# Optimization experiments

Measured on AMD Instinct MI355X. Metric: run time of the kernel, lower is better.

Reference implementation:

```python
import jax, jax.numpy as jnp
import numpy as np

E = 1024
H = 16
HD = 64
DI = E // 16  # 64, GRU hidden size
VOCAB = 32000
B, T = 2, 2048


def adaptive_pool_matrix(l_in, l_out):
    # PyTorch AdaptiveAvgPool1d: out[i] = mean(in[floor(i*l_in/l_out) : ceil((i+1)*l_in/l_out)])
    P = np.zeros((l_in, l_out), np.float32)
    for i in range(l_out):
        s = (i * l_in) // l_out
        e = -((-(i + 1) * l_in) // l_out)
        P[s:e, i] = 1.0 / (e - s)
    return jnp.asarray(P)


def gru(x, wih, whh):
    # x: [B, T, DI]; wih/whh: [3*DI, DI]; no bias; gate order (r, z, n)
    h_dim = whh.shape[1]
    xw = jnp.einsum('btd,gd->btg', x, wih)  # [B, T, 3*DI]

    def step(h, xw_t):
        hw = h @ whh.T
        r = jax.nn.sigmoid(xw_t[:, :h_dim] + hw[:, :h_dim])
        z = jax.nn.sigmoid(xw_t[:, h_dim:2 * h_dim] + hw[:, h_dim:2 * h_dim])
        n = jnp.tanh(xw_t[:, 2 * h_dim:] + r * hw[:, 2 * h_dim:])
        h_new = (1.0 - z) * n + z * h
        return h_new, h_new

    h0 = jnp.zeros((x.shape[0], h_dim), x.dtype)
    _, hs = jax.lax.scan(step, h0, jnp.swapaxes(xw, 0, 1))
    return jnp.swapaxes(hs, 0, 1)  # [B, T, DI]


def pos_embed(x, gru_wih, gru_whh, lin_w, p_pos, p_proj):
    # x: [B, T, E]. Pools act on the feature dim (torch last-dim after permute).
    x_proj = x @ p_proj            # [B, T, E-DI]
    pos = gru(x @ p_pos, gru_wih, gru_whh)  # [B, T, DI]
    out = jnp.concatenate([pos, x_proj], axis=-1) @ lin_w.T
    return out + x


def layernorm(x, w, b, eps=1e-5):
    mu = jnp.mean(x, axis=-1, keepdims=True)
    var = jnp.var(x, axis=-1, keepdims=True)
    return (x - mu) * jax.lax.rsqrt(var + eps) * w + b


def setup_inputs() -> dict:
    key = jax.random.key(0)
    ks = jax.random.split(key, 16)
    s = 0.02
    return {
        'x': jax.random.normal(ks[0], (B, T, E), jnp.float32),
        'token_ids': jax.random.randint(ks[1], (B, T), 0, VOCAB, jnp.int32),
        'q_gru_wih': jax.random.normal(ks[2], (3 * DI, DI), jnp.float32) * s,
        'q_gru_whh': jax.random.normal(ks[3], (3 * DI, DI), jnp.float32) * s,
        'q_lin_w': jax.random.normal(ks[4], (E, E), jnp.float32) * s,
        'k_gru_wih': jax.random.normal(ks[5], (3 * DI, DI), jnp.float32) * s,
        'k_gru_whh': jax.random.normal(ks[6], (3 * DI, DI), jnp.float32) * s,
        'k_lin_w': jax.random.normal(ks[7], (E, E), jnp.float32) * s,
        'v_emb': jax.random.normal(ks[8], (VOCAB, E), jnp.float32) * s + 1.0,
        'q_ln_w': jnp.ones((E,), jnp.float32),
        'q_ln_b': jnp.zeros((E,), jnp.float32),
        'k_ln_w': jnp.ones((E,), jnp.float32),
        'k_ln_b': jnp.zeros((E,), jnp.float32),
        'out_w': jax.random.normal(ks[9], (E, E), jnp.float32) * s,
        'out_b': jnp.zeros((E,), jnp.float32),
    }


def reference(x, token_ids, q_gru_wih, q_gru_whh, q_lin_w, k_gru_wih, k_gru_whh,
              k_lin_w, v_emb, q_ln_w, q_ln_b, k_ln_w, k_ln_b, out_w, out_b):
    p_pos = adaptive_pool_matrix(E, DI)
    p_proj = adaptive_pool_matrix(E, E - DI)

    q = pos_embed(x, q_gru_wih, q_gru_whh, q_lin_w, p_pos, p_proj)
    k = pos_embed(x, k_gru_wih, k_gru_whh, k_lin_w, p_pos, p_proj)
    v = jax.nn.silu(x) * v_emb[token_ids]  # [B, T, E]

    q = layernorm(q, q_ln_w, q_ln_b)
    k = layernorm(k, k_ln_w, k_ln_b)

    # [B, T, E] -> [B, H, T, HD]
    def split_heads(t):
        return t.reshape(B, T, H, HD).transpose(0, 2, 1, 3)

    qh, kh, vh = split_heads(q), split_heads(k), split_heads(v)

    scores = jnp.einsum('bhtd,bhsd->bhts', qh, kh) / jnp.sqrt(jnp.float32(HD))
    # Original code: attn_weights += attn_weights.masked_fill(mask, -inf)
    # => unmasked scores are DOUBLED; masked (future) positions become -inf.
    causal = jnp.triu(jnp.ones((T, T), bool), k=1)  # True above diagonal
    scores = jnp.where(causal, -jnp.inf, scores * 2.0)
    attn = jax.nn.softmax(scores, axis=-1)

    out = jnp.einsum('bhts,bhsd->bhtd', attn, vh)  # [B, H, T, HD]
    out = out.transpose(0, 2, 1, 3).reshape(B, T, E)
    return out @ out_w.T + out_b
```

## Files before the change

kernel.cpp:

```cpp
#include <hip/hip_runtime.h>


namespace {

constexpr int B_ = 2, T_ = 2048, E_ = 1024, H_ = 16, HD_ = 64, G3_ = 192, M_ = B_ * T_;

typedef _Float16 f16;
typedef _Float16 f16x8 __attribute__((ext_vector_type(8)));
typedef _Float16 f16x4 __attribute__((ext_vector_type(4)));
typedef _Float16 f16x2 __attribute__((ext_vector_type(2)));
typedef float f32x4 __attribute__((ext_vector_type(4)));

__device__ __forceinline__ f32x4 mfma16(f16x8 a, f16x8 b, f32x4 c) {
  return __builtin_amdgcn_mfma_f32_16x16x32_f16(a, b, c, 0, 0, 0);
}

#if __has_builtin(__builtin_amdgcn_fdot2)
__device__ __forceinline__ float fdot2(f16x2 a, f16x2 b, float c) {
  return __builtin_amdgcn_fdot2(a, b, c, false);
}
#else
__device__ __forceinline__ float fdot2(f16x2 a, f16x2 b, float c) {
  return c + (float)a[0] * (float)b[0] + (float)a[1] * (float)b[1];
}
#endif

__global__ __launch_bounds__(256) void k_cvt(const float* __restrict__ s,
                                             f16* __restrict__ d, int n) {
  int i = (blockIdx.x * 256 + threadIdx.x) * 4;
  if (i < n) {
    float4 v = *(const float4*)(s + i);
    f16x4 o = {(f16)v.x, (f16)v.y, (f16)v.z, (f16)v.w};
    *(f16x4*)(d + i) = o;
  }
}

__global__ __launch_bounds__(256) void k_prep(
    const float* __restrict__ x, const int* __restrict__ tok,
    const f16* __restrict__ wihq, const f16* __restrict__ wihk,
    const float* __restrict__ v_emb,
    f16* __restrict__ vh, f16* __restrict__ aq, f16* __restrict__ ak,
    float* __restrict__ xwq, float* __restrict__ xwk) {
  __shared__ float xs[E_];
  __shared__ float xp[64];
  const int row = blockIdx.x;
  const int b = row >> 11, t = row & (T_ - 1);
  const int tid = threadIdx.x;
  const float* xrow = x + (size_t)row * E_;
  {
    const int tk = tok[row];
    float4 xv = ((const float4*)xrow)[tid];
    ((float4*)xs)[tid] = xv;
    float4 ev = ((const float4*)(v_emb + (size_t)tk * E_))[tid];
    f16x4 o;
    o[0] = (f16)(xv.x / (1.f + __expf(-xv.x)) * ev.x);
    o[1] = (f16)(xv.y / (1.f + __expf(-xv.y)) * ev.y);
    o[2] = (f16)(xv.z / (1.f + __expf(-xv.z)) * ev.z);
    o[3] = (f16)(xv.w / (1.f + __expf(-xv.w)) * ev.w);
    const int e0 = tid * 4;
    const size_t voff = ((size_t)(b * H_ + (e0 >> 6)) * T_ + t) * HD_ + (e0 & 63);
    *(f16x4*)(vh + voff) = o;
  }
  __syncthreads();
  if (tid < 64) {
    float s = 0.f;
#pragma unroll
    for (int j = 0; j < 16; ++j) s += xs[tid * 16 + j];
    xp[tid] = s * (1.f / 16.f);
  }
  for (int i = tid; i < 960; i += 256) {
    int s0 = (i * 1024) / 960;
    int e0 = ((i + 1) * 1024 + 959) / 960;
    float m = xs[s0];
    if (e0 - s0 == 2) m = (m + xs[s0 + 1]) * 0.5f;
    f16 hv = (f16)m;
    aq[(size_t)row * E_ + 64 + i] = hv;
    ak[(size_t)row * E_ + 64 + i] = hv;
  }
  __syncthreads();
  for (int o = tid; o < 2 * G3_; o += 256) {
    const int chain = o / G3_, g = o % G3_;
    const f16* wrow = (chain ? wihk : wihq) + g * 64;
    float acc = 0.f;
#pragma unroll
    for (int c = 0; c < 8; ++c) {
      f16x8 wv = *(const f16x8*)(wrow + c * 8);
#pragma unroll
      for (int u = 0; u < 8; ++u) acc += xp[c * 8 + u] * (float)wv[u];
    }
    (chain ? xwk : xwq)[(size_t)row * G3_ + g] = acc;
  }
}

__global__ __launch_bounds__(64, 1) void k_gru(
    const float* __restrict__ xwq, const float* __restrict__ xwk,
    const float* __restrict__ whhq, const float* __restrict__ whhk,
    f16* __restrict__ aq, f16* __restrict__ ak) {
  const int blk = blockIdx.x;
  const int chain = blk >> 1, b = blk & 1;
  const float* xw = (chain ? xwk : xwq) + (size_t)b * T_ * G3_;
  const float* whh = chain ? whhk : whhq;
  f16* a = (chain ? ak : aq) + (size_t)b * T_ * E_;
  const int j = threadIdx.x;
  f16x2 wr2[32], wz2[32], wn2[32];
#pragma unroll
  for (int i = 0; i < 32; ++i) {
    float2 r2 = *(const float2*)(whh + (size_t)j * 64 + 2 * i);
    float2 z2 = *(const float2*)(whh + (size_t)(64 + j) * 64 + 2 * i);
    float2 n2 = *(const float2*)(whh + (size_t)(128 + j) * 64 + 2 * i);
    wr2[i] = {(f16)r2.x, (f16)r2.y};
    wz2[i] = {(f16)z2.x, (f16)z2.y};
    wn2[i] = {(f16)n2.x, (f16)n2.y};
  }
  float h = 0.f;
  float xr = xw[j], xz = xw[64 + j], xn = xw[128 + j];
  for (int t = 0; t < T_; ++t) {
    const f16 h16 = (f16)h;
    const unsigned hu = (unsigned)__builtin_bit_cast(unsigned short, h16);
    const unsigned nb = (unsigned)__shfl_xor((int)hu, 1) & 0xffffu;
    const unsigned pk = (j & 1) ? (nb | (hu << 16)) : (hu | (nb << 16));
    int hp[32];
#pragma unroll
    for (int i = 0; i < 32; ++i) hp[i] = __builtin_amdgcn_readlane((int)pk, 2 * i);
    const int tn = (t + 1 < T_) ? (t + 1) : (T_ - 1);
    const float* xp2 = xw + (size_t)tn * G3_;
    const float nxr = xp2[j], nxz = xp2[64 + j], nxn = xp2[128 + j];
    float ar = 0.f, az = 0.f, an = 0.f;
#pragma unroll
    for (int i = 0; i < 32; ++i) {
      const f16x2 hh = __builtin_bit_cast(f16x2, hp[i]);
      ar = fdot2(wr2[i], hh, ar);
      az = fdot2(wz2[i], hh, az);
      an = fdot2(wn2[i], hh, an);
    }
    const float r = 1.f / (1.f + __expf(-(xr + ar)));
    const float z = 1.f / (1.f + __expf(-(xz + az)));
    const float pre = xn + r * an;
    const float ea = __expf(-2.f * fabsf(pre));
    float nn = (1.f - ea) / (1.f + ea);
    nn = copysignf(nn, pre);
    h = (1.f - z) * nn + z * h;
    a[(size_t)t * E_ + j] = (f16)h;
    xr = nxr; xz = nxz; xn = nxn;
  }
}

template <int MODE>
__global__ __launch_bounds__(256) void k_gemm(
    const f16* __restrict__ A, const f16* __restrict__ W,
    const float* __restrict__ add, const float* __restrict__ bias,
    float* __restrict__ C) {
  __shared__ __align__(16) f16 As[128][72];
  __shared__ __align__(16) f16 Bs[128][72];
  const int m0 = blockIdx.x * 128, n0 = blockIdx.y * 128;
  const int tid = threadIdx.x;
  const int wid = tid >> 6, lane = tid & 63;
  const int wr = wid >> 1, wc = wid & 1;
  const int lg = lane >> 4, lc = lane & 15;
  f32x4 acc[4][4] = {};
  for (int kt = 0; kt < E_; kt += 64) {
#pragma unroll
    for (int it = 0; it < 4; ++it) {
      const int r = it * 32 + (tid >> 3);
      const int cs = (tid & 7) * 8;
      *(f16x8*)&As[r][cs] = *(const f16x8*)(A + (size_t)(m0 + r) * E_ + kt + cs);
      *(f16x8*)&Bs[r][cs] = *(const f16x8*)(W + (size_t)(n0 + r) * E_ + kt + cs);
    }
    __syncthreads();
    f16x8 af[4][2], bf[4][2];
#pragma unroll
    for (int mi = 0; mi < 4; ++mi)
#pragma unroll
      for (int ks = 0; ks < 2; ++ks) {
        af[mi][ks] = *(const f16x8*)&As[wr * 64 + mi * 16 + lc][ks * 32 + lg * 8];
        bf[mi][ks] = *(const f16x8*)&Bs[wc * 64 + mi * 16 + lc][ks * 32 + lg * 8];
      }
#pragma unroll
    for (int mi = 0; mi < 4; ++mi)
#pragma unroll
      for (int ni = 0; ni < 4; ++ni)
#pragma unroll
        for (int ks = 0; ks < 2; ++ks)
          acc[mi][ni] = mfma16(af[mi][ks], bf[ni][ks], acc[mi][ni]);
    __syncthreads();
  }
#pragma unroll
  for (int mi = 0; mi < 4; ++mi) {
    const int r0 = m0 + wr * 64 + mi * 16 + lg * 4;
#pragma unroll
    for (int ni = 0; ni < 4; ++ni) {
      const int col = n0 + wc * 64 + ni * 16 + lc;
      const float bv = (MODE == 1) ? bias[col] : 0.f;
#pragma unroll
      for (int q = 0; q < 4; ++q) {
        float v = acc[mi][ni][q];
        if (MODE == 0) v += add[(size_t)(r0 + q) * E_ + col];
        else v += bv;
        C[(size_t)(r0 + q) * E_ + col] = v;
      }
    }
  }
}

__global__ __launch_bounds__(256) void k_ln(const float* __restrict__ pre,
                                            const float* __restrict__ gw,
                                            const float* __restrict__ gb,
                                            f16* __restrict__ outp) {
  const int row = blockIdx.x;
  const int tid = threadIdx.x;
  const float4 v = ((const float4*)(pre + (size_t)row * E_))[tid];
  float s = v.x + v.y + v.z + v.w;
  float s2 = v.x * v.x + v.y * v.y + v.z * v.z + v.w * v.w;
#pragma unroll
  for (int off = 32; off; off >>= 1) {
    s += __shfl_xor(s, off);
    s2 += __shfl_xor(s2, off);
  }
  __shared__ float red[8];
  const int wid = tid >> 6, lane = tid & 63;
  if (!lane) { red[wid] = s; red[4 + wid] = s2; }
  __syncthreads();
  s = red[0] + red[1] + red[2] + red[3];
  s2 = red[4] + red[5] + red[6] + red[7];
  const float mu = s * (1.f / E_);
  const float inv = rsqrtf(s2 * (1.f / E_) - mu * mu + 1e-5f);
  const float4 w4 = ((const float4*)gw)[tid];
  const float4 b4 = ((const float4*)gb)[tid];
  const int e0 = tid * 4;
  f16x4 o;
  o[0] = (f16)((v.x - mu) * inv * w4.x + b4.x);
  o[1] = (f16)((v.y - mu) * inv * w4.y + b4.y);
  o[2] = (f16)((v.z - mu) * inv * w4.z + b4.z);
  o[3] = (f16)((v.w - mu) * inv * w4.w + b4.w);
  const int b = row >> 11, t = row & (T_ - 1);
  const size_t off2 = ((size_t)(b * H_ + (e0 >> 6)) * T_ + t) * HD_ + (e0 & 63);
  *(f16x4*)(outp + off2) = o;
}

__global__ __launch_bounds__(256) void k_attn(const f16* __restrict__ Q,
                                              const f16* __restrict__ K,
                                              const f16* __restrict__ V,
                                              f16* __restrict__ AO) {
  __shared__ __align__(16) f16 Kt[64][72];
  __shared__ __align__(16) f16 Vt[64][72];
  __shared__ __align__(16) f16 Ps[4][16][72];
  const int qi = blockIdx.x, bh = blockIdx.y;
  const int b = bh >> 4, h = bh & 15;
  const int tid = threadIdx.x, wid = tid >> 6, lane = tid & 63;
  const int lg = lane >> 4, lc = lane & 15;
  const size_t hbase = (size_t)bh * T_ * HD_;
  const int qb = qi * 64;
  f16x8 qf[2];
  {
    const int qrow = qb + wid * 16 + lc;
#pragma unroll
    for (int ks = 0; ks < 2; ++ks)
      qf[ks] = *(const f16x8*)(Q + hbase + (size_t)qrow * HD_ + ks * 32 + lg * 8);
  }
  f32x4 o[4] = {};
  float m_run[4] = {-1e30f, -1e30f, -1e30f, -1e30f};
  float l_run[4] = {};
  const int qrow_d = qb + wid * 16 + lg * 4;
  for (int kt = 0; kt <= qi; ++kt) {
    {
      const int r = tid >> 2, cs = (tid & 3) * 16;
      const f16* ksrc = K + hbase + (size_t)(kt * 64 + r) * HD_ + cs;
      *(f16x8*)&Kt[r][cs] = *(const f16x8*)ksrc;
      *(f16x8*)&Kt[r][cs + 8] = *(const f16x8*)(ksrc + 8);
      const f16* vsrc = V + hbase + (size_t)(kt * 64 + lane) * HD_ + wid * 16;
      f16x8 va = *(const f16x8*)vsrc;
      f16x8 vb = *(const f16x8*)(vsrc + 8);
#pragma unroll
      for (int u = 0; u < 8; ++u) {
        Vt[wid * 16 + u][lane] = va[u];
        Vt[wid * 16 + 8 + u][lane] = vb[u];
      }
    }
    __syncthreads();
    f32x4 s[4] = {};
#pragma unroll
    for (int nt = 0; nt < 4; ++nt)
#pragma unroll
      for (int ks = 0; ks < 2; ++ks) {
        f16x8 kf = *(const f16x8*)&Kt[nt * 16 + lc][ks * 32 + lg * 8];
        s[nt] = mfma16(qf[ks], kf, s[nt]);
      }
    const bool diag = (kt == qi);
#pragma unroll
    for (int nt = 0; nt < 4; ++nt) {
      const int colg = kt * 64 + nt * 16 + lc;
#pragma unroll
      for (int r = 0; r < 4; ++r) {
        float v = s[nt][r] * 0.25f;
        if (diag && colg > qrow_d + r) v = -1e30f;
        s[nt][r] = v;
      }
    }
    float scalev[4];
#pragma unroll
    for (int r = 0; r < 4; ++r) {
      float m = fmaxf(fmaxf(s[0][r], s[1][r]), fmaxf(s[2][r], s[3][r]));
#pragma unroll
      for (int of = 1; of < 16; of <<= 1) m = fmaxf(m, __shfl_xor(m, of));
      const float mn = fmaxf(m_run[r], m);
      scalev[r] = __expf(m_run[r] - mn);
      m_run[r] = mn;
    }
    float ladd[4] = {};
#pragma unroll
    for (int nt = 0; nt < 4; ++nt)
#pragma unroll
      for (int r = 0; r < 4; ++r) {
        const float p = __expf(s[nt][r] - m_run[r]);
        s[nt][r] = p;
        ladd[r] += p;
      }
#pragma unroll
    for (int r = 0; r < 4; ++r) {
      float la = ladd[r];
#pragma unroll
      for (int of = 1; of < 16; of <<= 1) la += __shfl_xor(la, of);
      l_run[r] = l_run[r] * scalev[r] + la;
      o[0][r] *= scalev[r];
      o[1][r] *= scalev[r];
      o[2][r] *= scalev[r];
      o[3][r] *= scalev[r];
    }
#pragma unroll
    for (int nt = 0; nt < 4; ++nt)
#pragma unroll
      for (int r = 0; r < 4; ++r)
        Ps[wid][lg * 4 + r][nt * 16 + lc] = (f16)s[nt][r];
    f16x8 pf[2];
#pragma unroll
    for (int ks = 0; ks < 2; ++ks)
      pf[ks] = *(const f16x8*)&Ps[wid][lc][ks * 32 + lg * 8];
#pragma unroll
    for (int nt = 0; nt < 4; ++nt)
#pragma unroll
      for (int ks = 0; ks < 2; ++ks) {
        f16x8 vf = *(const f16x8*)&Vt[nt * 16 + lc][ks * 32 + lg * 8];
        o[nt] = mfma16(pf[ks], vf, o[nt]);
      }
    __syncthreads();
  }
#pragma unroll
  for (int nt = 0; nt < 4; ++nt)
#pragma unroll
    for (int r = 0; r < 4; ++r) {
      const float val = o[nt][r] / l_run[r];
      const int qrow = qrow_d + r;
      AO[((size_t)(b * T_ + qrow)) * E_ + h * HD_ + nt * 16 + lc] = (f16)val;
    }
}

}

extern "C" void kernel_launch(void* const* d_in, const int* in_sizes, int n_in,
                              void* d_out, int out_size, void* d_ws, size_t ws_size,
                              hipStream_t stream) {
  (void)in_sizes; (void)n_in; (void)out_size; (void)ws_size;
  const float* x      = (const float*)d_in[0];
  const int*   tok    = (const int*)d_in[1];
  const float* q_wih  = (const float*)d_in[2];
  const float* q_whh  = (const float*)d_in[3];
  const float* q_lin  = (const float*)d_in[4];
  const float* k_wih  = (const float*)d_in[5];
  const float* k_whh  = (const float*)d_in[6];
  const float* k_lin  = (const float*)d_in[7];
  const float* v_emb  = (const float*)d_in[8];
  const float* q_ln_w = (const float*)d_in[9];
  const float* q_ln_b = (const float*)d_in[10];
  const float* k_ln_w = (const float*)d_in[11];
  const float* k_ln_b = (const float*)d_in[12];
  const float* out_w  = (const float*)d_in[13];
  const float* out_b  = (const float*)d_in[14];
  float* outp = (float*)d_out;

  char* ws = (char*)d_ws;
  size_t off = 0;
  auto take = [&](size_t bytes) -> void* {
    void* p = ws + off;
    off += (bytes + 255) & ~(size_t)255;
    return p;
  };
  f16* WQ   = (f16*)take((size_t)E_ * E_ * 2);
  f16* WK   = (f16*)take((size_t)E_ * E_ * 2);
  f16* WO   = (f16*)take((size_t)E_ * E_ * 2);
  f16* WIHQ = (f16*)take((size_t)G3_ * 64 * 2);
  f16* WIHK = (f16*)take((size_t)G3_ * 64 * 2);
  f16* AQ   = (f16*)take((size_t)M_ * E_ * 2);
  f16* AK   = (f16*)take((size_t)M_ * E_ * 2);
  f16* VH   = (f16*)take((size_t)M_ * E_ * 2);
  f16* QH   = (f16*)take((size_t)M_ * E_ * 2);
  f16* KH   = (f16*)take((size_t)M_ * E_ * 2);
  f16* AO   = (f16*)take((size_t)M_ * E_ * 2);
  float* XWQ  = (float*)take((size_t)M_ * G3_ * 4);
  float* XWK  = (float*)take((size_t)M_ * G3_ * 4);
  float* QPRE = (float*)take((size_t)M_ * E_ * 4);
  float* KPRE = (float*)take((size_t)M_ * E_ * 4);

  k_cvt<<<dim3((E_ * E_) / 1024), dim3(256), 0, stream>>>(q_lin, WQ, E_ * E_);
  k_cvt<<<dim3((E_ * E_) / 1024), dim3(256), 0, stream>>>(k_lin, WK, E_ * E_);
  k_cvt<<<dim3((E_ * E_) / 1024), dim3(256), 0, stream>>>(out_w, WO, E_ * E_);
  k_cvt<<<dim3((G3_ * 64) / 1024), dim3(256), 0, stream>>>(q_wih, WIHQ, G3_ * 64);
  k_cvt<<<dim3((G3_ * 64) / 1024), dim3(256), 0, stream>>>(k_wih, WIHK, G3_ * 64);

  k_prep<<<dim3(M_), dim3(256), 0, stream>>>(x, tok, WIHQ, WIHK, v_emb, VH, AQ, AK, XWQ, XWK);
  k_gru<<<dim3(4), dim3(64), 0, stream>>>(XWQ, XWK, q_whh, k_whh, AQ, AK);

  k_gemm<0><<<dim3(M_ / 128, E_ / 128), dim3(256), 0, stream>>>(AQ, WQ, x, nullptr, QPRE);
  k_gemm<0><<<dim3(M_ / 128, E_ / 128), dim3(256), 0, stream>>>(AK, WK, x, nullptr, KPRE);
  k_ln<<<dim3(M_), dim3(256), 0, stream>>>(QPRE, q_ln_w, q_ln_b, QH);
  k_ln<<<dim3(M_), dim3(256), 0, stream>>>(KPRE, k_ln_w, k_ln_b, KH);

  k_attn<<<dim3(T_ / 64, B_ * H_), dim3(256), 0, stream>>>(QH, KH, VH, AO);
  k_gemm<1><<<dim3(M_ / 128, E_ / 128), dim3(256), 0, stream>>>(AO, WO, nullptr, out_b, outp);
}
```

Baseline: 1.084 ms.

## Overlap GRU recurrence with pooled-feature GEMM in one mega kernel

Merges the serial GRU scan with the Q/K projection GEMMs and the out_w fp16 conversion into one launch. Block 0 runs all four GRU chains as four waves, while the other blocks compute the GEMM over the K range that skips the first 64 GRU columns. A later k_fix kernel adds the GRU-column contribution and the residual x. The GRU step is also reworked: gate weights are prescaled so sigmoid/tanh become exp2 plus rcp, lanes are broadcast via permlane32 swap, and the three dot products are reordered to shorten the dependency chain. The Q/K LayerNorms are batched into one launch. The cost is an extra read-modify-write pass over QPRE/KPRE and a dependence on GEMM blocks co-running with the long GRU block, since k_mega does not return until the GRU finishes.

```diff
diff --git a/kernel.cpp b/kernel.cpp
--- a/kernel.cpp
+++ b/kernel.cpp
@@ -4,6 +4,8 @@
 namespace {
 
 constexpr int B_ = 2, T_ = 2048, E_ = 1024, H_ = 16, HD_ = 64, G3_ = 192, M_ = B_ * T_;
+constexpr float SRg = -1.4426950408889634f;
+constexpr float SNg = 2.8853900817779268f;
 
 typedef _Float16 f16;
 typedef _Float16 f16x8 __attribute__((ext_vector_type(8)));
@@ -24,6 +26,21 @@
   return c + (float)a[0] * (float)b[0] + (float)a[1] * (float)b[1];
 }
 #endif
+
+__device__ __forceinline__ float exp2_(float x) {
+#if __has_builtin(__builtin_amdgcn_exp2f)
+  return __builtin_amdgcn_exp2f(x);
+#else
+  return exp2f(x);
+#endif
+}
+__device__ __forceinline__ float rcp_(float x) {
+#if __has_builtin(__builtin_amdgcn_rcpf)
+  return __builtin_amdgcn_rcpf(x);
+#else
+  return 1.f / x;
+#endif
+}
 
 __global__ __launch_bounds__(256) void k_cvt(const float* __restrict__ s,
                                              f16* __restrict__ d, int n) {
@@ -88,124 +105,204 @@
 #pragma unroll
       for (int u = 0; u < 8; ++u) acc += xp[c * 8 + u] * (float)wv[u];
     }
-    (chain ? xwk : xwq)[(size_t)row * G3_ + g] = acc;
-  }
-}
-
-__global__ __launch_bounds__(64, 1) void k_gru(
+    const float sc = (g < 128) ? SRg : SNg;
+    (chain ? xwk : xwq)[(size_t)row * G3_ + g] = acc * sc;
+  }
+}
+
+__device__ __forceinline__ void gru_core(const float* __restrict__ xw,
+                                         const float* __restrict__ whh,
+                                         f16* __restrict__ a, int lane) {
+  f16x2 wr[32], wz[32], wn[32];
+#pragma unroll
+  for (int i = 0; i < 32; ++i) {
+    wr[i] = {(f16)(whh[(size_t)lane * 64 + i] * SRg),
+             (f16)(whh[(size_t)lane * 64 + i + 32] * SRg)};
+    wz[i] = {(f16)(whh[(size_t)(64 + lane) * 64 + i] * SRg),
+             (f16)(whh[(size_t)(64 + lane) * 64 + i + 32] * SRg)};
+    wn[i] = {(f16)(whh[(size_t)(128 + lane) * 64 + i] * SNg),
+             (f16)(whh[(size_t)(128 + lane) * 64 + i + 32] * SNg)};
+  }
+  float h = 0.f;
+  float xr = xw[lane], xz = xw[64 + lane], xn = xw[128 + lane];
+  for (int t = 0; t < T_; ++t) {
+    const unsigned hu = (unsigned)__builtin_bit_cast(unsigned short, (f16)h);
+    int va = (int)hu, vb = (int)hu;
+    asm volatile("v_permlane32_swap_b32 %0, %1" : "+v"(va), "+v"(vb));
+    const int pk = (int)(hu | ((unsigned)va << 16));
+    int hp[32];
+#pragma unroll
+    for (int i = 0; i < 32; ++i) hp[i] = __builtin_amdgcn_readlane(pk, i);
+    const int tn = (t + 1 < T_) ? t + 1 : t;
+    const float* nx = xw + (size_t)tn * G3_;
+    const float nxr = nx[lane], nxz = nx[64 + lane], nxn = nx[128 + lane];
+    float ar = xr;
+#pragma unroll
+    for (int i = 0; i < 32; ++i)
+      ar = fdot2(wr[i], __builtin_bit_cast(f16x2, hp[i]), ar);
+    const float r = rcp_(1.f + exp2_(ar));
+    float an = 0.f;
+#pragma unroll
+    for (int i = 0; i < 32; ++i)
+      an = fdot2(wn[i], __builtin_bit_cast(f16x2, hp[i]), an);
+    const float p2 = fmaf(r, an, xn);
+    const float n = fmaf(-2.f, rcp_(1.f + exp2_(p2)), 1.f);
+    float az = xz;
+#pragma unroll
+    for (int i = 0; i < 32; ++i)
+      az = fdot2(wz[i], __builtin_bit_cast(f16x2, hp[i]), az);
+    const float z = rcp_(1.f + exp2_(az));
+    h = fmaf(z, h - n, n);
+    a[(size_t)t * E_ + lane] = (f16)h;
+    xr = nxr; xz = nxz; xn = nxn;
+  }
+}
+
+__global__ __launch_bounds__(256, 1) void k_mega(
     const float* __restrict__ xwq, const float* __restrict__ xwk,
     const float* __restrict__ whhq, const float* __restrict__ whhk,
-    f16* __restrict__ aq, f16* __restrict__ ak) {
-  const int blk = blockIdx.x;
-  const int chain = blk >> 1, b = blk & 1;
-  const float* xw = (chain ? xwk : xwq) + (size_t)b * T_ * G3_;
-  const float* whh = chain ? whhk : whhq;
-  f16* a = (chain ? ak : aq) + (size_t)b * T_ * E_;
-  const int j = threadIdx.x;
-  f16x2 wr2[32], wz2[32], wn2[32];
-#pragma unroll
-  for (int i = 0; i < 32; ++i) {
-    float2 r2 = *(const float2*)(whh + (size_t)j * 64 + 2 * i);
-    float2 z2 = *(const float2*)(whh + (size_t)(64 + j) * 64 + 2 * i);
-    float2 n2 = *(const float2*)(whh + (size_t)(128 + j) * 64 + 2 * i);
-    wr2[i] = {(f16)r2.x, (f16)r2.y};
-    wz2[i] = {(f16)z2.x, (f16)z2.y};
-    wn2[i] = {(f16)n2.x, (f16)n2.y};
-  }
-  float h = 0.f;
-  float xr = xw[j], xz = xw[64 + j], xn = xw[128 + j];
-  for (int t = 0; t < T_; ++t) {
-    const f16 h16 = (f16)h;
-    const unsigned hu = (unsigned)__builtin_bit_cast(unsigned short, h16);
-    const unsigned nb = (unsigned)__shfl_xor((int)hu, 1) & 0xffffu;
-    const unsigned pk = (j & 1) ? (nb | (hu << 16)) : (hu | (nb << 16));
-    int hp[32];
-#pragma unroll
-    for (int i = 0; i < 32; ++i) hp[i] = __builtin_amdgcn_readlane((int)pk, 2 * i);
-    const int tn = (t + 1 < T_) ? (t + 1) : (T_ - 1);
-    const float* xp2 = xw + (size_t)tn * G3_;
-    const float nxr = xp2[j], nxz = xp2[64 + j], nxn = xp2[128 + j];
-    float ar = 0.f, az = 0.f, an = 0.f;
-#pragma unroll
-    for (int i = 0; i < 32; ++i) {
-      const f16x2 hh = __builtin_bit_cast(f16x2, hp[i]);
-      ar = fdot2(wr2[i], hh, ar);
-      az = fdot2(wz2[i], hh, az);
-      an = fdot2(wn2[i], hh, an);
-    }
-    const float r = 1.f / (1.f + __expf(-(xr + ar)));
-    const float z = 1.f / (1.f + __expf(-(xz + az)));
-    const float pre = xn + r * an;
-    const float ea = __expf(-2.f * fabsf(pre));
-    float nn = (1.f - ea) / (1.f + ea);
-    nn = copysignf(nn, pre);
-    h = (1.f - z) * nn + z * h;
-    a[(size_t)t * E_ + j] = (f16)h;
-    xr = nxr; xz = nxz; xn = nxn;
-  }
-}
-
-template <int MODE>
-__global__ __launch_bounds__(256) void k_gemm(
-    const f16* __restrict__ A, const f16* __restrict__ W,
-    const float* __restrict__ add, const float* __restrict__ bias,
-    float* __restrict__ C) {
+    f16* __restrict__ aq, f16* __restrict__ ak,
+    const f16* __restrict__ WQ, const f16* __restrict__ WK,
+    float* __restrict__ QPRE, float* __restrict__ KPRE,
+    const float* __restrict__ out_w, f16* __restrict__ WO) {
   __shared__ __align__(16) f16 As[128][72];
   __shared__ __align__(16) f16 Bs[128][72];
+  const int bx = blockIdx.x;
+  const int tid = threadIdx.x;
+  if (bx == 0) {
+    const int wid = tid >> 6, lane = tid & 63;
+    const int qk = wid >> 1, b = wid & 1;
+    const float* xw = (qk ? xwk : xwq) + (size_t)b * T_ * G3_;
+    const float* whh = qk ? whhk : whhq;
+    f16* a = (qk ? ak : aq) + (size_t)b * T_ * E_;
+    gru_core(xw, whh, a, lane);
+    return;
+  }
+  if (bx <= 512) {
+    const int bid = bx - 1;
+    const int chain = bid >> 8, tile = bid & 255;
+    const int m0 = (tile >> 3) * 128, n0 = (tile & 7) * 128;
+    const f16* A = chain ? ak : aq;
+    const f16* W = chain ? WK : WQ;
+    float* C = chain ? KPRE : QPRE;
+    const int wid = tid >> 6, lane = tid & 63;
+    const int wr = wid >> 1, wc = wid & 1;
+    const int lg = lane >> 4, lc = lane & 15;
+    f32x4 acc[4][4] = {};
+    for (int kt = 64; kt < E_; kt += 64) {
+#pragma unroll
+      for (int it = 0; it < 4; ++it) {
+        const int r = it * 32 + (tid >> 3);
+        const int cs = (tid & 7) * 8;
+        *(f16x8*)&As[r][cs] = *(const f16x8*)(A + (size_t)(m0 + r) * E_ + kt + cs);
+        *(f16x8*)&Bs[r][cs] = *(const f16x8*)(W + (size_t)(n0 + r) * E_ + kt + cs);
+      }
+      __syncthreads();
+      f16x8 af[4][2], bf[4][2];
+#pragma unroll
+      for (int mi = 0; mi < 4; ++mi)
+#pragma unroll
+        for (int ks = 0; ks < 2; ++ks) {
+          af[mi][ks] = *(const f16x8*)&As[wr * 64 + mi * 16 + lc][ks * 32 + lg * 8];
+          bf[mi][ks] = *(const f16x8*)&Bs[wc * 64 + mi * 16 + lc][ks * 32 + lg * 8];
+        }
+#pragma unroll
+      for (int mi = 0; mi < 4; ++mi)
+#pragma unroll
+        for (int ni = 0; ni < 4; ++ni)
+#pragma unroll
+          for (int ks = 0; ks < 2; ++ks)
+            acc[mi][ni] = mfma16(af[mi][ks], bf[ni][ks], acc[mi][ni]);
+      __syncthreads();
+    }
+#pragma unroll
+    for (int mi = 0; mi < 4; ++mi) {
+      const int r0 = m0 + wr * 64 + mi * 16 + lg * 4;
+#pragma unroll
+      for (int ni = 0; ni < 4; ++ni) {
+        const int col = n0 + wc * 64 + ni * 16 + lc;
+#pragma unroll
+        for (int q = 0; q < 4; ++q)
+          C[(size_t)(r0 + q) * E_ + col] = acc[mi][ni][q];
+      }
+    }
+    return;
+  }
+  {
+    const int cb = bx - 513;
+    for (int i = cb * 256 + tid; i < E_ * E_ / 4; i += 8 * 256) {
+      float4 v = ((const float4*)out_w)[i];
+      f16x4 o = {(f16)v.x, (f16)v.y, (f16)v.z, (f16)v.w};
+      *(f16x4*)(WO + (size_t)i * 4) = o;
+    }
+  }
+}
+
+__global__ __launch_bounds__(256) void k_fix(
+    const f16* __restrict__ aq, const f16* __restrict__ ak,
+    const f16* __restrict__ WQ, const f16* __restrict__ WK,
+    const float* __restrict__ x, float* __restrict__ QPRE,
+    float* __restrict__ KPRE) {
+  __shared__ __align__(16) f16 As[128][72];
+  __shared__ __align__(16) f16 Bs[128][72];
+  const int chain = blockIdx.z;
+  const f16* A = chain ? ak : aq;
+  const f16* W = chain ? WK : WQ;
+  float* C = chain ? KPRE : QPRE;
   const int m0 = blockIdx.x * 128, n0 = blockIdx.y * 128;
   const int tid = threadIdx.x;
   const int wid = tid >> 6, lane = tid & 63;
   const int wr = wid >> 1, wc = wid & 1;
   const int lg = lane >> 4, lc = lane & 15;
+#pragma unroll
+  for (int it = 0; it < 4; ++it) {
+    const int r = it * 32 + (tid >> 3);
+    const int cs = (tid & 7) * 8;
+    *(f16x8*)&As[r][cs] = *(const f16x8*)(A + (size_t)(m0 + r) * E_ + cs);
+    *(f16x8*)&Bs[r][cs] = *(const f16x8*)(W + (size_t)(n0 + r) * E_ + cs);
+  }
+  __syncthreads();
   f32x4 acc[4][4] = {};
-  for (int kt = 0; kt < E_; kt += 64) {
-#pragma unroll
-    for (int it = 0; it < 4; ++it) {
-      const int r = it * 32 + (tid >> 3);
-      const int cs = (tid & 7) * 8;
-      *(f16x8*)&As[r][cs] = *(const f16x8*)(A + (size_t)(m0 + r) * E_ + kt + cs);
-      *(f16x8*)&Bs[r][cs] = *(const f16x8*)(W + (size_t)(n0 + r) * E_ + kt + cs);
-    }
-    __syncthreads();
-    f16x8 af[4][2], bf[4][2];
-#pragma unroll
-    for (int mi = 0; mi < 4; ++mi)
-#pragma unroll
-      for (int ks = 0; ks < 2; ++ks) {
-        af[mi][ks] = *(const f16x8*)&As[wr * 64 + mi * 16 + lc][ks * 32 + lg * 8];
-        bf[mi][ks] = *(const f16x8*)&Bs[wc * 64 + mi * 16 + lc][ks * 32 + lg * 8];
-      }
-#pragma unroll
-    for (int mi = 0; mi < 4; ++mi)
-#pragma unroll
-      for (int ni = 0; ni < 4; ++ni)
-#pragma unroll
-        for (int ks = 0; ks < 2; ++ks)
-          acc[mi][ni] = mfma16(af[mi][ks], bf[ni][ks], acc[mi][ni]);
-    __syncthreads();
-  }
+  f16x8 af[4][2], bf[4][2];
+#pragma unroll
+  for (int mi = 0; mi < 4; ++mi)
+#pragma unroll
+    for (int ks = 0; ks < 2; ++ks) {
+      af[mi][ks] = *(const f16x8*)&As[wr * 64 + mi * 16 + lc][ks * 32 + lg * 8];
+      bf[mi][ks] = *(const f16x8*)&Bs[wc * 64 + mi * 16 + lc][ks * 32 + lg * 8];
+    }
+#pragma unroll
+  for (int mi = 0; mi < 4; ++mi)
+#pragma unroll
+    for (int ni = 0; ni < 4; ++ni)
+#pragma unroll
+      for (int ks = 0; ks < 2; ++ks)
+        acc[mi][ni] = mfma16(af[mi][ks], bf[ni][ks], acc[mi][ni]);
 #pragma unroll
   for (int mi = 0; mi < 4; ++mi) {
     const int r0 = m0 + wr * 64 + mi * 16 + lg * 4;
 #pragma unroll
     for (int ni = 0; ni < 4; ++ni) {
       const int col = n0 + wc * 64 + ni * 16 + lc;
-      const float bv = (MODE == 1) ? bias[col] : 0.f;
 #pragma unroll
       for (int q = 0; q < 4; ++q) {
-        float v = acc[mi][ni][q];
-        if (MODE == 0) v += add[(size_t)(r0 + q) * E_ + col];
-        else v += bv;
-        C[(size_t)(r0 + q) * E_ + col] = v;
-      }
-    }
-  }
-}
-
-__global__ __launch_bounds__(256) void k_ln(const float* __restrict__ pre,
-                                            const float* __restrict__ gw,
-                                            const float* __restrict__ gb,
-                                            f16* __restrict__ outp) {
+        const size_t idx = (size_t)(r0 + q) * E_ + col;
+        C[idx] += acc[mi][ni][q] + x[idx];
+      }
+    }
+  }
+}
+
+__global__ __launch_bounds__(256) void k_ln(
+    const float* __restrict__ qpre, const float* __restrict__ kpre,
+    const float* __restrict__ qw, const float* __restrict__ qb,
+    const float* __restrict__ kw, const float* __restrict__ kb,
+    f16* __restrict__ qh, f16* __restrict__ kh) {
+  const int chain = blockIdx.y;
+  const float* pre = chain ? kpre : qpre;
+  const float* gw = chain ? kw : qw;
+  const float* gb = chain ? kb : qb;
+  f16* outp = chain ? kh : qh;
   const int row = blockIdx.x;
   const int tid = threadIdx.x;
   const float4 v = ((const float4*)(pre + (size_t)row * E_))[tid];
@@ -352,6 +449,57 @@
       const int qrow = qrow_d + r;
       AO[((size_t)(b * T_ + qrow)) * E_ + h * HD_ + nt * 16 + lc] = (f16)val;
     }
+}
+
+__global__ __launch_bounds__(256) void k_gemm_out(
+    const f16* __restrict__ A, const f16* __restrict__ W,
+    const float* __restrict__ bias, float* __restrict__ C) {
+  __shared__ __align__(16) f16 As[128][72];
+  __shared__ __align__(16) f16 Bs[128][72];
+  const int m0 = blockIdx.x * 128, n0 = blockIdx.y * 128;
+  const int tid = threadIdx.x;
+  const int wid = tid >> 6, lane = tid & 63;
+  const int wr = wid >> 1, wc = wid & 1;
+  const int lg = lane >> 4, lc = lane & 15;
+  f32x4 acc[4][4] = {};
+  for (int kt = 0; kt < E_; kt += 64) {
+#pragma unroll
+    for (int it = 0; it < 4; ++it) {
+      const int r = it * 32 + (tid >> 3);
+      const int cs = (tid & 7) * 8;
+      *(f16x8*)&As[r][cs] = *(const f16x8*)(A + (size_t)(m0 + r) * E_ + kt + cs);
+      *(f16x8*)&Bs[r][cs] = *(const f16x8*)(W + (size_t)(n0 + r) * E_ + kt + cs);
+    }
+    __syncthreads();
+    f16x8 af[4][2], bf[4][2];
+#pragma unroll
+    for (int mi = 0; mi < 4; ++mi)
+#pragma unroll
+      for (int ks = 0; ks < 2; ++ks) {
+        af[mi][ks] = *(const f16x8*)&As[wr * 64 + mi * 16 + lc][ks * 32 + lg * 8];
+        bf[mi][ks] = *(const f16x8*)&Bs[wc * 64 + mi * 16 + lc][ks * 32 + lg * 8];
+      }
+#pragma unroll
+    for (int mi = 0; mi < 4; ++mi)
+#pragma unroll
+      for (int ni = 0; ni < 4; ++ni)
+#pragma unroll
+        for (int ks = 0; ks < 2; ++ks)
+          acc[mi][ni] = mfma16(af[mi][ks], bf[ni][ks], acc[mi][ni]);
+    __syncthreads();
+  }
+#pragma unroll
+  for (int mi = 0; mi < 4; ++mi) {
+    const int r0 = m0 + wr * 64 + mi * 16 + lg * 4;
+#pragma unroll
+    for (int ni = 0; ni < 4; ++ni) {
+      const int col = n0 + wc * 64 + ni * 16 + lc;
+      const float bv = bias[col];
+#pragma unroll
+      for (int q = 0; q < 4; ++q)
+        C[(size_t)(r0 + q) * E_ + col] = acc[mi][ni][q] + bv;
+    }
+  }
 }
 
 }
@@ -402,18 +550,17 @@
 
   k_cvt<<<dim3((E_ * E_) / 1024), dim3(256), 0, stream>>>(q_lin, WQ, E_ * E_);
   k_cvt<<<dim3((E_ * E_) / 1024), dim3(256), 0, stream>>>(k_lin, WK, E_ * E_);
-  k_cvt<<<dim3((E_ * E_) / 1024), dim3(256), 0, stream>>>(out_w, WO, E_ * E_);
   k_cvt<<<dim3((G3_ * 64) / 1024), dim3(256), 0, stream>>>(q_wih, WIHQ, G3_ * 64);
   k_cvt<<<dim3((G3_ * 64) / 1024), dim3(256), 0, stream>>>(k_wih, WIHK, G3_ * 64);
 
   k_prep<<<dim3(M_), dim3(256), 0, stream>>>(x, tok, WIHQ, WIHK, v_emb, VH, AQ, AK, XWQ, XWK);
-  k_gru<<<dim3(4), dim3(64), 0, stream>>>(XWQ, XWK, q_whh, k_whh, AQ, AK);
-
-  k_gemm<0><<<dim3(M_ / 128, E_ / 128), dim3(256), 0, stream>>>(AQ, WQ, x, nullptr, QPRE);
-  k_gemm<0><<<dim3(M_ / 128, E_ / 128), dim3(256), 0, stream>>>(AK, WK, x, nullptr, KPRE);
-  k_ln<<<dim3(M_), dim3(256), 0, stream>>>(QPRE, q_ln_w, q_ln_b, QH);
-  k_ln<<<dim3(M_), dim3(256), 0, stream>>>(KPRE, k_ln_w, k_ln_b, KH);
+
+  k_mega<<<dim3(521), dim3(256), 0, stream>>>(XWQ, XWK, q_whh, k_whh, AQ, AK,
+                                              WQ, WK, QPRE, KPRE, out_w, WO);
+
+  k_fix<<<dim3(M_ / 128, E_ / 128, 2), dim3(256), 0, stream>>>(AQ, AK, WQ, WK, x, QPRE, KPRE);
+  k_ln<<<dim3(M_, 2), dim3(256), 0, stream>>>(QPRE, KPRE, q_ln_w, q_ln_b, k_ln_w, k_ln_b, QH, KH);
 
   k_attn<<<dim3(T_ / 64, B_ * H_), dim3(256), 0, stream>>>(QH, KH, VH, AO);
-  k_gemm<1><<<dim3(M_ / 128, E_ / 128), dim3(256), 0, stream>>>(AO, WO, nullptr, out_b, outp);
-}
+  k_gemm_out<<<dim3(M_ / 128, E_ / 128), dim3(256), 0, stream>>>(AO, WO, out_b, outp);
+}
```

Result: faster. 883.6 us (median of 4 runs) (-18.5%).
